# Kernel tuning notes

Hardware: AMD Instinct MI355X
Metric: run time of the kernel (lower is better)

Reference implementation:

```python
import jax, jax.numpy as jnp
import numpy as np

S, N, V, E, H, L = 40, 256, 32000, 1024, 1024, 2


def _gru_step(x, h, wih, whh, bih, bhh):
    # PyTorch GRU cell, gate order [r, z, n]
    gi = x @ wih.T + bih          # (N, 3H)
    gh = h @ whh.T + bhh          # (N, 3H)
    ir, iz, inn = jnp.split(gi, 3, axis=-1)
    hr, hz, hn = jnp.split(gh, 3, axis=-1)
    r = jax.nn.sigmoid(ir + hr)
    z = jax.nn.sigmoid(iz + hz)
    n = jnp.tanh(inn + r * hn)
    return (1.0 - z) * n + z * h


def setup_inputs() -> dict:
    key = jax.random.key(0)
    ks = jax.random.split(key, 16)
    nrm = lambda k, shp: (jax.random.normal(k, shp, jnp.float32) * 0.05)
    return {
        "tokens": jax.random.randint(ks[0], (S, N), 0, V),
        "hidden": jnp.zeros((L, N, H), jnp.float32),
        "emb": nrm(ks[1], (V, E)),
        "enc_wih": nrm(ks[2], (L, 3 * H, E)),
        "enc_whh": nrm(ks[3], (L, 3 * H, H)),
        "enc_bih": nrm(ks[4], (L, 3 * H)),
        "enc_bhh": nrm(ks[5], (L, 3 * H)),
        "dec_wih": nrm(ks[6], (L, 3 * H, H)),
        "dec_whh": nrm(ks[7], (L, 3 * H, H)),
        "dec_bih": nrm(ks[8], (L, 3 * H)),
        "dec_bhh": nrm(ks[9], (L, 3 * H)),
        "attn_w": nrm(ks[10], (S, E + L * H)),
        "attn_b": nrm(ks[11], (S,)),
        "comb_w": nrm(ks[12], (H, 2 * H)),
        "comb_b": nrm(ks[13], (H,)),
    }


def reference(tokens, hidden, emb, enc_wih, enc_whh, enc_bih, enc_bhh,
              dec_wih, dec_whh, dec_bih, dec_bhh,
              attn_w, attn_b, comb_w, comb_b):
    x = emb[tokens]                      # (S, N, E) embedded input

    # ---- encoder: 2-layer GRU over the full sequence ----
    seq = x
    h_finals = []
    for l in range(L):
        wih, whh, bih, bhh = enc_wih[l], enc_whh[l], enc_bih[l], enc_bhh[l]
        def step(h, xt, wih=wih, whh=whh, bih=bih, bhh=bhh):
            h2 = _gru_step(xt, h, wih, whh, bih, bhh)
            return h2, h2
        hT, seq = jax.lax.scan(step, hidden[l], seq)
        h_finals.append(hT)
    h_n = jnp.stack(h_finals)            # (L, N, H)
    enc_out = jnp.swapaxes(seq, 0, 1)    # (N, S, H)

    # ---- attention decoder: scan over timesteps, carry decoder hidden ----
    def dec_step(h, emb_t):
        # h: (L, N, H), emb_t: (N, E)
        h_flat = jnp.swapaxes(h, 0, 1).reshape(N, L * H)
        logits = jnp.concatenate([emb_t, h_flat], axis=-1) @ attn_w.T + attn_b
        aw = jax.nn.softmax(logits, axis=-1)                   # (N, S)
        applied = jnp.einsum('ns,nsh->nh', aw, enc_out)        # (N, H)
        xcur = jax.nn.relu(
            jnp.concatenate([emb_t, applied], axis=-1) @ comb_w.T + comb_b)
        hs = []
        for l in range(L):
            hl = _gru_step(xcur, h[l], dec_wih[l], dec_whh[l],
                           dec_bih[l], dec_bhh[l])
            hs.append(hl)
            xcur = hl
        return jnp.stack(hs), xcur

    hT, outs = jax.lax.scan(dec_step, h_n, x)   # outs: (S, N, H)
    return outs, hT
```

## Files before the change

kernel.cpp:

```cpp
#include <hip/hip_runtime.h>
#include <hip/hip_bf16.h>

#define S_LEN 40
#define NB    256
#define EDIM  1024
#define HDIM  1024
#define NBLK  256
#define NTHR  768

typedef _Float16 f16;
typedef __attribute__((ext_vector_type(8))) _Float16 f16x8;
typedef __attribute__((ext_vector_type(4))) _Float16 f16x4;
typedef __attribute__((ext_vector_type(4))) float f32x4;

__device__ __forceinline__ float sigm(float x) {
    x = fminf(fmaxf(x, -30.f), 30.f);
    return 1.f / (1.f + __expf(-x));
}
__device__ __forceinline__ float tanh_fast(float x) {
    x = fminf(fmaxf(x, -15.f), 15.f);
    float e = __expf(2.f * x);
    return (e - 1.f) / (e + 1.f);
}

__device__ __forceinline__ void sysld_issue_b128(f16x8& v, const void* p) {
    asm volatile("global_load_dwordx4 %0, %1, off sc0 sc1" : "=v"(v) : "v"(p));
}
__device__ __forceinline__ void sysld_issue_f32(float& v, const void* p) {
    asm volatile("global_load_dword %0, %1, off sc0 sc1" : "=v"(v) : "v"(p));
}
__device__ __forceinline__ void sysld_issue_f32x4(f32x4& v, const void* p) {
    asm volatile("global_load_dwordx4 %0, %1, off sc0 sc1" : "=v"(v) : "v"(p));
}
__device__ __forceinline__ void sys_wait() {
    asm volatile("s_waitcnt vmcnt(0)" ::: "memory");
    __builtin_amdgcn_sched_barrier(0);
}
__device__ __forceinline__ void sysst_f32(float* p, float v) {
    asm volatile("global_store_dword %0, %1, off sc0 sc1" :: "v"(p), "v"(v) : "memory");
}
__device__ __forceinline__ void sysst_f32x4(float* p, f32x4 v) {
    asm volatile("global_store_dwordx4 %0, %1, off sc0 sc1" :: "v"(p), "v"(v) : "memory");
}
__device__ __forceinline__ void sysst_f16(f16* p, f16 v) {
    union { f16 f; unsigned short s; } u; u.f = v;
    unsigned int b = u.s;
    asm volatile("global_store_short %0, %1, off sc0 sc1" :: "v"(p), "v"(b) : "memory");
}

__device__ __forceinline__ void gbar(unsigned* cnt, unsigned* gen) {
    asm volatile("s_waitcnt vmcnt(0)" ::: "memory");
    __syncthreads();
    if (threadIdx.x == 0) {
        unsigned g = __hip_atomic_load(gen, __ATOMIC_RELAXED, __HIP_MEMORY_SCOPE_AGENT);
        unsigned a = __hip_atomic_fetch_add(cnt, 1u, __ATOMIC_RELEASE, __HIP_MEMORY_SCOPE_AGENT);
        if (a == NBLK - 1) {
            __hip_atomic_store(cnt, 0u, __ATOMIC_RELAXED, __HIP_MEMORY_SCOPE_AGENT);
            __hip_atomic_fetch_add(gen, 1u, __ATOMIC_RELEASE, __HIP_MEMORY_SCOPE_AGENT);
        } else {
            while (__hip_atomic_load(gen, __ATOMIC_RELAXED, __HIP_MEMORY_SCOPE_AGENT) == g)
                __builtin_amdgcn_s_sleep(2);
        }
    }
    __syncthreads();
}

__global__ void k_init_sync(unsigned* s) { s[0] = 0; s[1] = 0; }

__device__ __forceinline__ void probe_mn(int lane, int* mrow, int* ncol) {
    f16x8 pa, pb;
#pragma unroll
    for (int e = 0; e < 8; e++) {
        pa[e] = (f16)(float)(lane & 15);
        pb[e] = (f16)0.03125f;
    }
    f32x4 pacc = {0, 0, 0, 0};
    pacc = __builtin_amdgcn_mfma_f32_16x16x32_f16(pa, pb, pacc, 0, 0, 0);
#pragma unroll
    for (int r = 0; r < 4; r++) {
        int m = (int)(pacc[r] + 0.5f);
        int cg = ((lane >> 4) << 2) + r;
        mrow[r] = m;
        ncol[r] = (m == cg) ? (lane & 15) : cg;
    }
}

__global__ __launch_bounds__(256) void k_cvt4(const float* __restrict__ src,
                                              f16* __restrict__ dst, int n4) {
    int i = blockIdx.x * 256 + threadIdx.x;
    if (i < n4) {
        f32x4 v = ((const f32x4*)src)[i];
        f16x4 o = {(f16)v.x, (f16)v.y, (f16)v.z, (f16)v.w};
        ((f16x4*)dst)[i] = o;
    }
}
__global__ __launch_bounds__(256) void k_copyf4(const float* __restrict__ src,
                                                float* __restrict__ dst, int n4) {
    int i = blockIdx.x * 256 + threadIdx.x;
    if (i < n4) ((f32x4*)dst)[i] = ((const f32x4*)src)[i];
}
__global__ __launch_bounds__(256) void k_embed_cvt(const int* __restrict__ tok,
                                                   const float* __restrict__ emb,
                                                   f16* __restrict__ xe) {
    int b = blockIdx.x;
    int t = threadIdx.x;
    int token = tok[b];
    f32x4 v = ((const f32x4*)(emb + (size_t)token * EDIM))[t];
    f16x4 o = {(f16)v.x, (f16)v.y, (f16)v.z, (f16)v.w};
    ((f16x4*)(xe + (size_t)b * EDIM))[t] = o;
}

__device__ void gru_phase(
    char* lds, int bid, int tid, const int* mr, const int* nc,
    const f16* __restrict__ xsrc, bool xsys,
    const f16* __restrict__ hsrc, const float* __restrict__ hfsrc,
    const f16* __restrict__ wih, const f16* __restrict__ whh,
    const float* __restrict__ bih, const float* __restrict__ bhh,
    f16* ho16, float* hof, f16* o216, float* o2f) {
    const int cb = (bid & 31) * 32;
    const int rb = (bid >> 5) * 32;

    {
        constexpr int TOT = 8192;
        constexpr int IT = (TOT + NTHR - 1) / NTHR;
        f16x8 val[IT];
#pragma unroll
        for (int i = 0; i < IT; i++) {
            int c = tid + i * NTHR;
            if (c < TOT) {
                int isH = c >> 12;
                int cl = c & 4095;
                int row = cl >> 7, cc = cl & 127;
                const f16* src = (isH ? hsrc : xsrc) +
                                 (size_t)(rb + row) * 1024 + cc * 8;
                if (isH || xsys) sysld_issue_b128(val[i], src);
                else             val[i] = *(const f16x8*)src;
            }
        }
        sys_wait();
#pragma unroll
        for (int i = 0; i < IT; i++) {
            int c = tid + i * NTHR;
            if (c < TOT) {
                int isH = c >> 12;
                int cl = c & 4095;
                int row = cl >> 7, cc = cl & 127;
                *(f16x8*)(lds + isH * 65536 + row * 2048 +
                          ((cc ^ (row & 7)) << 4)) = val[i];
            }
        }
    }
    __syncthreads();

    const int w = tid >> 6, lane = tid & 63;
    const int pair = w >> 1, kh = w & 1;
    const int gate = (pair >= 3) ? pair - 3 : pair;
    const int r0 = lane & 15, kk0 = (lane >> 4) * 8;
    const f16* B = ((pair < 3) ? wih : whh) + ((size_t)gate * HDIM + cb) * 1024;
    const f16* B0 = B + (size_t)r0 * 1024 + kk0 + kh * 512;
    const f16* B1 = B + (size_t)(r0 + 16) * 1024 + kk0 + kh * 512;
    const int abase = (pair < 3) ? 0 : 65536;
    const int swz = r0 & 7;
    const char* a0p = lds + abase + r0 * 2048;
    const char* a1p = lds + abase + (r0 + 16) * 2048;

    f32x4 acc00 = {0,0,0,0}, acc01 = {0,0,0,0}, acc10 = {0,0,0,0}, acc11 = {0,0,0,0};
#pragma unroll 4
    for (int k = 0; k < 512; k += 32) {
        int g = (kh * 512 + kk0 + k) >> 3;
        int off = (g ^ swz) << 4;
        f16x8 a0 = *(const f16x8*)(a0p + off);
        f16x8 a1 = *(const f16x8*)(a1p + off);
        f16x8 b0 = *(const f16x8*)(B0 + k);
        f16x8 b1 = *(const f16x8*)(B1 + k);
        acc00 = __builtin_amdgcn_mfma_f32_16x16x32_f16(a0, b0, acc00, 0, 0, 0);
        acc01 = __builtin_amdgcn_mfma_f32_16x16x32_f16(a0, b1, acc01, 0, 0, 0);
        acc10 = __builtin_amdgcn_mfma_f32_16x16x32_f16(a1, b0, acc10, 0, 0, 0);
        acc11 = __builtin_amdgcn_mfma_f32_16x16x32_f16(a1, b1, acc11, 0, 0, 0);
    }
    __syncthreads();

    float* red = (float*)lds;
    float* rw = red + w * 1024;
#pragma unroll
    for (int r = 0; r < 4; r++) {
        rw[mr[r] * 32 + nc[r]]             = acc00[r];
        rw[mr[r] * 32 + nc[r] + 16]        = acc01[r];
        rw[(mr[r] + 16) * 32 + nc[r]]      = acc10[r];
        rw[(mr[r] + 16) * 32 + nc[r] + 16] = acc11[r];
    }
    __syncthreads();

    {
        float hp[2];
#pragma unroll
        for (int it = 0; it < 2; it++) {
            int i = tid + it * NTHR;
            if (i < 1024) {
                int rr = i >> 5, ccn = i & 31;
                sysld_issue_f32(hp[it], hfsrc + (size_t)(rb + rr) * HDIM + cb + ccn);
            }
        }
        sys_wait();
#pragma unroll
        for (int it = 0; it < 2; it++) {
            int i = tid + it * NTHR;
            if (i < 1024) {
                int rr = i >> 5, ccn = i & 31;
                int col = cb + ccn;
                int row = rb + rr;
                float gir = red[i]         + red[1024 + i];
                float giz = red[2048 + i]  + red[3072 + i];
                float gin = red[4096 + i]  + red[5120 + i];
                float ghr = red[6144 + i]  + red[7168 + i];
                float ghz = red[8192 + i]  + red[9216 + i];
                float ghn = red[10240 + i] + red[11264 + i];
                float r = sigm(gir + bih[col] + ghr + bhh[col]);
                float z = sigm(giz + bih[HDIM + col] + ghz + bhh[HDIM + col]);
                float n = tanh_fast(gin + bih[2 * HDIM + col] +
                                    r * (ghn + bhh[2 * HDIM + col]));
                float hn2 = (1.f - z) * n + z * hp[it];
                size_t idx = (size_t)row * HDIM + col;
                sysst_f16(ho16 + idx, (f16)hn2);
                sysst_f32(hof + idx, hn2);
                if (o216) sysst_f16(o216 + idx, (f16)hn2);
                if (o2f)  sysst_f32(o2f + idx, hn2);
            }
        }
    }
}

__device__ void attn_phase(
    char* lds, int bid, int tid,
    const f16* __restrict__ xe_t, const f16* __restrict__ h0,
    const f16* __restrict__ h1,
    const f16* __restrict__ attn_w, const float* __restrict__ attn_b,
    const f16* __restrict__ enc16, f16* __restrict__ appl) {
    float* logit = (float*)(lds + 131072);
    float* awls  = logit + 64;
    const int n = bid;
    const int w = tid >> 6, lane = tid & 63;

    {
        constexpr int TOT = 5504;
        constexpr int IT = (TOT + NTHR - 1) / NTHR;
        f16x8 val[IT];
#pragma unroll
        for (int i = 0; i < IT; i++) {
            int c = tid + i * NTHR;
            if (c < TOT) {
                if (c < 5120) {
                    int s = c >> 7, cc = c & 127;
                    val[i] = *(const f16x8*)(enc16 + ((size_t)s * NB + n) * 1024 + cc * 8);
                } else {
                    int r = c - 5120;
                    if (r < 128) {
                        val[i] = *(const f16x8*)(xe_t + (size_t)n * 1024 + r * 8);
                    } else if (r < 256) {
                        sysld_issue_b128(val[i], h0 + (size_t)n * 1024 + (r - 128) * 8);
                    } else {
                        sysld_issue_b128(val[i], h1 + (size_t)n * 1024 + (r - 256) * 8);
                    }
                }
            }
        }
        sys_wait();
#pragma unroll
        for (int i = 0; i < IT; i++) {
            int c = tid + i * NTHR;
            if (c < TOT) {
                if (c < 5120) *(f16x8*)(lds + c * 16) = val[i];
                else          *(f16x8*)(lds + 81920 + (c - 5120) * 16) = val[i];
            }
        }
    }
    __syncthreads();

    if (w < 10) {
#pragma unroll
        for (int si = 0; si < 4; si++) {
            int s = w * 4 + si;
            const f16* wrow = attn_w + (size_t)s * 3072;
            float acc = 0.f;
#pragma unroll
            for (int jj = 0; jj < 6; jj++) {
                int j = lane + jj * 64;
                f16x8 a = *(const f16x8*)(lds + 81920 + j * 16);
                f16x8 b = *(const f16x8*)(wrow + j * 8);
#pragma unroll
                for (int e = 0; e < 8; e++)
                    acc = fmaf((float)a[e], (float)b[e], acc);
            }
            for (int o = 32; o; o >>= 1) acc += __shfl_down(acc, o);
            if (lane == 0) logit[s] = acc + attn_b[s];
        }
    }
    __syncthreads();

    if (w == 0) {
        float v = (lane < S_LEN) ? logit[lane] : -1e30f;
        float m = v;
        for (int o = 32; o; o >>= 1) m = fmaxf(m, __shfl_xor(m, o));
        float e = (lane < S_LEN) ? __expf(v - m) : 0.f;
        float sum = e;
        for (int o = 32; o; o >>= 1) sum += __shfl_xor(sum, o);
        if (lane < S_LEN) awls[lane] = e / sum;
    }
    __syncthreads();

    for (int col = tid; col < 1024; col += NTHR) {
        float acc = 0.f;
#pragma unroll
        for (int s = 0; s < S_LEN; s++)
            acc = fmaf(awls[s], (float)*(const f16*)(lds + s * 2048 + col * 2), acc);
        sysst_f16(appl + (size_t)n * 1024 + col, (f16)acc);
    }
}

__device__ void comb_phase(
    char* lds, int bid, int tid, const int* mr, const int* nc,
    const f16* __restrict__ xe_t, const f16* __restrict__ appl,
    const f16* __restrict__ Bw, const float* __restrict__ bias,
    f16* __restrict__ Cout) {
    const int cb = (bid & 31) * 32;
    const int rb = (bid >> 5) * 32;

    {
        constexpr int TOT = 8192;
        constexpr int IT = (TOT + NTHR - 1) / NTHR;
        f16x8 val[IT];
#pragma unroll
        for (int i = 0; i < IT; i++) {
            int c = tid + i * NTHR;
            if (c < TOT) {
                int row = c >> 8, cc = c & 255;
                if (cc < 128)
                    val[i] = *(const f16x8*)(xe_t + (size_t)(rb + row) * 1024 + cc * 8);
                else
                    sysld_issue_b128(val[i], appl + (size_t)(rb + row) * 1024 + (cc - 128) * 8);
            }
        }
        sys_wait();
#pragma unroll
        for (int i = 0; i < IT; i++) {
            int c = tid + i * NTHR;
            if (c < TOT) {
                int row = c >> 8, cc = c & 255;
                *(f16x8*)(lds + row * 4096 + ((cc ^ (row & 7)) << 4)) = val[i];
            }
        }
    }
    __syncthreads();

    const int w = tid >> 6, lane = tid & 63;
    const int r0 = lane & 15, kk0 = (lane >> 4) * 8;
    const int c0 = (w * 64) / 12, c1 = ((w + 1) * 64) / 12;
    const f16* B0 = Bw + (size_t)(cb + r0) * 2048 + kk0;
    const f16* B1 = Bw + (size_t)(cb + r0 + 16) * 2048 + kk0;
    const int swz = r0 & 7;
    const char* a0p = lds + r0 * 4096;
    const char* a1p = lds + (r0 + 16) * 4096;

    f32x4 acc00 = {0,0,0,0}, acc01 = {0,0,0,0}, acc10 = {0,0,0,0}, acc11 = {0,0,0,0};
    for (int c = c0; c < c1; c++) {
        int g = (c * 32 + kk0) >> 3;
        int off = (g ^ swz) << 4;
        f16x8 a0 = *(const f16x8*)(a0p + off);
        f16x8 a1 = *(const f16x8*)(a1p + off);
        f16x8 b0 = *(const f16x8*)(B0 + c * 32);
        f16x8 b1 = *(const f16x8*)(B1 + c * 32);
        acc00 = __builtin_amdgcn_mfma_f32_16x16x32_f16(a0, b0, acc00, 0, 0, 0);
        acc01 = __builtin_amdgcn_mfma_f32_16x16x32_f16(a0, b1, acc01, 0, 0, 0);
        acc10 = __builtin_amdgcn_mfma_f32_16x16x32_f16(a1, b0, acc10, 0, 0, 0);
        acc11 = __builtin_amdgcn_mfma_f32_16x16x32_f16(a1, b1, acc11, 0, 0, 0);
    }
    __syncthreads();

    float* red = (float*)lds;
    float* rw = red + w * 1024;
#pragma unroll
    for (int r = 0; r < 4; r++) {
        rw[mr[r] * 32 + nc[r]]             = acc00[r];
        rw[mr[r] * 32 + nc[r] + 16]        = acc01[r];
        rw[(mr[r] + 16) * 32 + nc[r]]      = acc10[r];
        rw[(mr[r] + 16) * 32 + nc[r] + 16] = acc11[r];
    }
    __syncthreads();

#pragma unroll
    for (int it = 0; it < 2; it++) {
        int i = tid + it * NTHR;
        if (i < 1024) {
            float s = 0.f;
#pragma unroll
            for (int p = 0; p < 12; p++) s += red[p * 1024 + i];
            int rr = i >> 5, ccn = i & 31;
            s += bias[cb + ccn];
            s = fmaxf(s, 0.f);
            sysst_f16(Cout + (size_t)(rb + rr) * 1024 + cb + ccn, (f16)s);
        }
    }
}

__global__ __launch_bounds__(NTHR, 3) void k_mega(
    const f16* __restrict__ xe,
    f16* h16, float* hf,
    const f16* __restrict__ w_eih, const f16* __restrict__ w_ehh,
    const float* __restrict__ enc_bih, const float* __restrict__ enc_bhh,
    const f16* __restrict__ w_dih, const f16* __restrict__ w_dhh,
    const float* __restrict__ dec_bih, const float* __restrict__ dec_bhh,
    const f16* __restrict__ w_attn, const float* __restrict__ attn_b,
    const f16* __restrict__ w_comb, const float* __restrict__ comb_b,
    f16* enc16, f16* appl, f16* xcur,
    float* out, unsigned* sync) {
    __shared__ char smem[131584];
    char* lds = smem;
    const int bid = blockIdx.x;
    const int tid = threadIdx.x;
    const int lane = tid & 63;
    const size_t NH = (size_t)NB * HDIM;

    int mr[4], nc[4];
    probe_mn(lane, mr, nc);

    unsigned* cnt = sync;
    unsigned* gen = sync + 1;

    f16* h0b[2] = { h16, h16 + 2 * NH };
    f16* h1b[2] = { h16 + NH, h16 + 3 * NH };
    float* h0f[2] = { hf, hf + 2 * NH };
    float* h1f[2] = { hf + NH, hf + 3 * NH };

    for (int t = 0; t < S_LEN; t++) {
        int p = t & 1;
        gru_phase(lds, bid, tid, mr, nc,
                  xe + (size_t)t * NB * EDIM, false,
                  h0b[p], h0f[p],
                  w_eih, w_ehh, enc_bih, enc_bhh,
                  h0b[p ^ 1], h0f[p ^ 1], (f16*)nullptr, (float*)nullptr);
        gbar(cnt, gen);
        gru_phase(lds, bid, tid, mr, nc,
                  h0b[p ^ 1], true,
                  h1b[p], h1f[p],
                  w_eih + (size_t)3 * HDIM * EDIM, w_ehh + (size_t)3 * HDIM * HDIM,
                  enc_bih + 3 * HDIM, enc_bhh + 3 * HDIM,
                  h1b[p ^ 1], h1f[p ^ 1], enc16 + (size_t)t * NH, (float*)nullptr);
        gbar(cnt, gen);
    }

    for (int t = 0; t < S_LEN; t++) {
        int p = t & 1;
        attn_phase(lds, bid, tid,
                   xe + (size_t)t * NB * EDIM, h0b[p], h1b[p],
                   w_attn, attn_b, enc16, appl);
        gbar(cnt, gen);
        comb_phase(lds, bid, tid, mr, nc,
                   xe + (size_t)t * NB * EDIM, appl, w_comb, comb_b, xcur);
        gbar(cnt, gen);
        gru_phase(lds, bid, tid, mr, nc,
                  xcur, true,
                  h0b[p], h0f[p],
                  w_dih, w_dhh, dec_bih, dec_bhh,
                  h0b[p ^ 1], h0f[p ^ 1], (f16*)nullptr, (float*)nullptr);
        gbar(cnt, gen);
        gru_phase(lds, bid, tid, mr, nc,
                  h0b[p ^ 1], true,
                  h1b[p], h1f[p],
                  w_dih + (size_t)3 * HDIM * HDIM, w_dhh + (size_t)3 * HDIM * HDIM,
                  dec_bih + 3 * HDIM, dec_bhh + 3 * HDIM,
                  h1b[p ^ 1], h1f[p ^ 1], (f16*)nullptr, out + (size_t)t * NH);
        gbar(cnt, gen);
    }

    if (tid < 512) {
        size_t idx = (size_t)bid * 512 + tid;
        f32x4 v;
        sysld_issue_f32x4(v, hf + idx * 4);
        sys_wait();
        sysst_f32x4(out + (size_t)S_LEN * NH + idx * 4, v);
    }
}

extern "C" void kernel_launch(void* const* d_in, const int* in_sizes, int n_in,
                              void* d_out, int out_size, void* d_ws, size_t ws_size,
                              hipStream_t stream) {
    const int*   tokens   = (const int*)d_in[0];
    const float* hidden   = (const float*)d_in[1];
    const float* emb      = (const float*)d_in[2];
    const float* enc_wih  = (const float*)d_in[3];
    const float* enc_whh  = (const float*)d_in[4];
    const float* enc_bih  = (const float*)d_in[5];
    const float* enc_bhh  = (const float*)d_in[6];
    const float* dec_wih  = (const float*)d_in[7];
    const float* dec_whh  = (const float*)d_in[8];
    const float* dec_bih  = (const float*)d_in[9];
    const float* dec_bhh  = (const float*)d_in[10];
    const float* attn_w   = (const float*)d_in[11];
    const float* attn_b   = (const float*)d_in[12];
    const float* comb_w   = (const float*)d_in[13];
    const float* comb_b   = (const float*)d_in[14];
    float* out = (float*)d_out;

    const size_t NH = (size_t)NB * HDIM;
    const size_t WSZ = (size_t)2 * 3 * HDIM * EDIM;

    float* hf = (float*)d_ws;
    f16* wp = (f16*)(hf + 4 * NH);
    f16 *w_eih = wp;  wp += WSZ;
    f16 *w_ehh = wp;  wp += WSZ;
    f16 *w_dih = wp;  wp += WSZ;
    f16 *w_dhh = wp;  wp += WSZ;
    f16 *w_comb = wp; wp += (size_t)HDIM * 2048;
    f16 *w_attn = wp; wp += (size_t)S_LEN * 3072;
    f16 *xe = wp;     wp += (size_t)S_LEN * NB * EDIM;
    f16 *enc16 = wp;  wp += (size_t)S_LEN * NH;
    f16 *h16 = wp;    wp += 4 * NH;
    f16 *appl = wp;   wp += NH;
    f16 *xcur = wp;   wp += NH;
    unsigned* syncp = (unsigned*)((((uintptr_t)wp) + 255) & ~(uintptr_t)255);

    k_init_sync<<<1, 1, 0, stream>>>(syncp);

    k_cvt4<<<(int)(WSZ / 4 / 256), 256, 0, stream>>>(enc_wih, w_eih, (int)(WSZ / 4));
    k_cvt4<<<(int)(WSZ / 4 / 256), 256, 0, stream>>>(enc_whh, w_ehh, (int)(WSZ / 4));
    k_cvt4<<<(int)(WSZ / 4 / 256), 256, 0, stream>>>(dec_wih, w_dih, (int)(WSZ / 4));
    k_cvt4<<<(int)(WSZ / 4 / 256), 256, 0, stream>>>(dec_whh, w_dhh, (int)(WSZ / 4));
    k_cvt4<<<(int)(HDIM * 2048 / 4 / 256), 256, 0, stream>>>(comb_w, w_comb,
                                                             HDIM * 2048 / 4);
    k_cvt4<<<(S_LEN * 3072 / 4 + 255) / 256, 256, 0, stream>>>(attn_w, w_attn,
                                                               S_LEN * 3072 / 4);
    k_embed_cvt<<<S_LEN * NB, 256, 0, stream>>>(tokens, emb, xe);
    k_cvt4<<<(int)(2 * NH / 4 / 256), 256, 0, stream>>>(hidden, h16, (int)(2 * NH / 4));
    k_copyf4<<<(int)(2 * NH / 4 / 256), 256, 0, stream>>>(hidden, hf, (int)(2 * NH / 4));

    k_mega<<<NBLK, NTHR, 0, stream>>>(
        xe, h16, hf,
        w_eih, w_ehh, enc_bih, enc_bhh,
        w_dih, w_dhh, dec_bih, dec_bhh,
        w_attn, attn_b, w_comb, comb_b,
        enc16, appl, xcur, out, syncp);
}
```

Baseline: 6.495 ms.

## Use hierarchical per-XCD grid barrier and nontemporal system-scope loads/stores

The flat global barrier, where all 256 blocks hit one counter, becomes a two-level barrier. Blocks first arrive on a counter for their own XCD, read from the hardware register, and then one representative per XCD arrives on a global counter. Per-XCD block counts are found at startup with an extra bootstrap barrier. All system-scope loads and stores gain the nt hint, and the encoder-output reads in attention now use sc0 sc1 loads, so data written by other XCDs is seen coherently. The aim is less atomic contention per barrier, at the cost of a second atomic hop and more complex startup logic.

```diff
diff --git a/kernel.cpp b/kernel.cpp
--- a/kernel.cpp
+++ b/kernel.cpp
@@ -24,31 +24,31 @@
 }
 
 __device__ __forceinline__ void sysld_issue_b128(f16x8& v, const void* p) {
-    asm volatile("global_load_dwordx4 %0, %1, off sc0 sc1" : "=v"(v) : "v"(p));
+    asm volatile("global_load_dwordx4 %0, %1, off sc0 sc1 nt" : "=v"(v) : "v"(p));
 }
 __device__ __forceinline__ void sysld_issue_f32(float& v, const void* p) {
-    asm volatile("global_load_dword %0, %1, off sc0 sc1" : "=v"(v) : "v"(p));
+    asm volatile("global_load_dword %0, %1, off sc0 sc1 nt" : "=v"(v) : "v"(p));
 }
 __device__ __forceinline__ void sysld_issue_f32x4(f32x4& v, const void* p) {
-    asm volatile("global_load_dwordx4 %0, %1, off sc0 sc1" : "=v"(v) : "v"(p));
+    asm volatile("global_load_dwordx4 %0, %1, off sc0 sc1 nt" : "=v"(v) : "v"(p));
 }
 __device__ __forceinline__ void sys_wait() {
     asm volatile("s_waitcnt vmcnt(0)" ::: "memory");
     __builtin_amdgcn_sched_barrier(0);
 }
 __device__ __forceinline__ void sysst_f32(float* p, float v) {
-    asm volatile("global_store_dword %0, %1, off sc0 sc1" :: "v"(p), "v"(v) : "memory");
+    asm volatile("global_store_dword %0, %1, off sc0 sc1 nt" :: "v"(p), "v"(v) : "memory");
 }
 __device__ __forceinline__ void sysst_f32x4(float* p, f32x4 v) {
-    asm volatile("global_store_dwordx4 %0, %1, off sc0 sc1" :: "v"(p), "v"(v) : "memory");
+    asm volatile("global_store_dwordx4 %0, %1, off sc0 sc1 nt" :: "v"(p), "v"(v) : "memory");
 }
 __device__ __forceinline__ void sysst_f16(f16* p, f16 v) {
     union { f16 f; unsigned short s; } u; u.f = v;
     unsigned int b = u.s;
-    asm volatile("global_store_short %0, %1, off sc0 sc1" :: "v"(p), "v"(b) : "memory");
-}
-
-__device__ __forceinline__ void gbar(unsigned* cnt, unsigned* gen) {
+    asm volatile("global_store_short %0, %1, off sc0 sc1 nt" :: "v"(p), "v"(b) : "memory");
+}
+
+__device__ __forceinline__ void gbar1(unsigned* cnt, unsigned* gen) {
     asm volatile("s_waitcnt vmcnt(0)" ::: "memory");
     __syncthreads();
     if (threadIdx.x == 0) {
@@ -65,7 +65,37 @@
     __syncthreads();
 }
 
-__global__ void k_init_sync(unsigned* s) { s[0] = 0; s[1] = 0; }
+__device__ __forceinline__ void g2bar(unsigned* sync, unsigned xcd,
+                                      unsigned M, unsigned NX) {
+    asm volatile("s_waitcnt vmcnt(0)" ::: "memory");
+    __syncthreads();
+    if (threadIdx.x == 0) {
+        unsigned* ggen = sync;
+        unsigned* gcnt = sync + 1;
+        unsigned* xa = sync + 16 + xcd * 16;
+        unsigned g = __hip_atomic_load(ggen, __ATOMIC_RELAXED, __HIP_MEMORY_SCOPE_AGENT);
+        unsigned a = __hip_atomic_fetch_add(xa, 1u, __ATOMIC_RELEASE, __HIP_MEMORY_SCOPE_AGENT);
+        if (a == M - 1) {
+            __hip_atomic_store(xa, 0u, __ATOMIC_RELAXED, __HIP_MEMORY_SCOPE_AGENT);
+            unsigned b = __hip_atomic_fetch_add(gcnt, 1u, __ATOMIC_RELEASE, __HIP_MEMORY_SCOPE_AGENT);
+            if (b == NX - 1) {
+                __hip_atomic_store(gcnt, 0u, __ATOMIC_RELAXED, __HIP_MEMORY_SCOPE_AGENT);
+                __hip_atomic_fetch_add(ggen, 1u, __ATOMIC_RELEASE, __HIP_MEMORY_SCOPE_AGENT);
+            } else {
+                while (__hip_atomic_load(ggen, __ATOMIC_RELAXED, __HIP_MEMORY_SCOPE_AGENT) == g)
+                    __builtin_amdgcn_s_sleep(4);
+            }
+        } else {
+            while (__hip_atomic_load(ggen, __ATOMIC_RELAXED, __HIP_MEMORY_SCOPE_AGENT) == g)
+                __builtin_amdgcn_s_sleep(4);
+        }
+    }
+    __syncthreads();
+}
+
+__global__ void k_init_sync(unsigned* s) {
+    for (int k = threadIdx.x; k < 1024; k += 256) s[k] = 0;
+}
 
 __device__ __forceinline__ void probe_mn(int lane, int* mrow, int* ncol) {
     f16x8 pa, pb;
@@ -251,7 +281,7 @@
             if (c < TOT) {
                 if (c < 5120) {
                     int s = c >> 7, cc = c & 127;
-                    val[i] = *(const f16x8*)(enc16 + ((size_t)s * NB + n) * 1024 + cc * 8);
+                    sysld_issue_b128(val[i], enc16 + ((size_t)s * NB + n) * 1024 + cc * 8);
                 } else {
                     int r = c - 5120;
                     if (r < 128) {
@@ -414,6 +444,7 @@
     f16* enc16, f16* appl, f16* xcur,
     float* out, unsigned* sync) {
     __shared__ char smem[131584];
+    __shared__ unsigned s_meta[4];
     char* lds = smem;
     const int bid = blockIdx.x;
     const int tid = threadIdx.x;
@@ -423,8 +454,27 @@
     int mr[4], nc[4];
     probe_mn(lane, mr, nc);
 
-    unsigned* cnt = sync;
-    unsigned* gen = sync + 1;
+    if (tid == 0) {
+        unsigned x;
+        asm volatile("s_getreg_b32 %0, hwreg(20, 0, 32)" : "=s"(x));
+        x &= 7;
+        unsigned r = __hip_atomic_fetch_add(sync + 256 + x, 1u,
+                                            __ATOMIC_RELAXED, __HIP_MEMORY_SCOPE_AGENT);
+        s_meta[0] = x; s_meta[1] = r;
+    }
+    __syncthreads();
+    gbar1(sync + 512, sync + 513);
+    if (tid == 0) {
+        unsigned M = __hip_atomic_load(sync + 256 + s_meta[0],
+                                       __ATOMIC_RELAXED, __HIP_MEMORY_SCOPE_AGENT);
+        unsigned nx = 0;
+        for (int i = 0; i < 8; i++)
+            nx += (__hip_atomic_load(sync + 256 + i, __ATOMIC_RELAXED,
+                                     __HIP_MEMORY_SCOPE_AGENT) > 0) ? 1u : 0u;
+        s_meta[2] = M; s_meta[3] = nx;
+    }
+    __syncthreads();
+    const unsigned xcd = s_meta[0], M = s_meta[2], NX = s_meta[3];
 
     f16* h0b[2] = { h16, h16 + 2 * NH };
     f16* h1b[2] = { h16 + NH, h16 + 3 * NH };
@@ -438,14 +488,14 @@
                   h0b[p], h0f[p],
                   w_eih, w_ehh, enc_bih, enc_bhh,
                   h0b[p ^ 1], h0f[p ^ 1], (f16*)nullptr, (float*)nullptr);
-        gbar(cnt, gen);
+        g2bar(sync, xcd, M, NX);
         gru_phase(lds, bid, tid, mr, nc,
                   h0b[p ^ 1], true,
                   h1b[p], h1f[p],
                   w_eih + (size_t)3 * HDIM * EDIM, w_ehh + (size_t)3 * HDIM * HDIM,
                   enc_bih + 3 * HDIM, enc_bhh + 3 * HDIM,
                   h1b[p ^ 1], h1f[p ^ 1], enc16 + (size_t)t * NH, (float*)nullptr);
-        gbar(cnt, gen);
+        g2bar(sync, xcd, M, NX);
     }
 
     for (int t = 0; t < S_LEN; t++) {
@@ -453,23 +503,23 @@
         attn_phase(lds, bid, tid,
                    xe + (size_t)t * NB * EDIM, h0b[p], h1b[p],
                    w_attn, attn_b, enc16, appl);
-        gbar(cnt, gen);
+        g2bar(sync, xcd, M, NX);
         comb_phase(lds, bid, tid, mr, nc,
                    xe + (size_t)t * NB * EDIM, appl, w_comb, comb_b, xcur);
-        gbar(cnt, gen);
+        g2bar(sync, xcd, M, NX);
         gru_phase(lds, bid, tid, mr, nc,
                   xcur, true,
                   h0b[p], h0f[p],
                   w_dih, w_dhh, dec_bih, dec_bhh,
                   h0b[p ^ 1], h0f[p ^ 1], (f16*)nullptr, (float*)nullptr);
-        gbar(cnt, gen);
+        g2bar(sync, xcd, M, NX);
         gru_phase(lds, bid, tid, mr, nc,
                   h0b[p ^ 1], true,
                   h1b[p], h1f[p],
                   w_dih + (size_t)3 * HDIM * HDIM, w_dhh + (size_t)3 * HDIM * HDIM,
                   dec_bih + 3 * HDIM, dec_bhh + 3 * HDIM,
                   h1b[p ^ 1], h1f[p ^ 1], (f16*)nullptr, out + (size_t)t * NH);
-        gbar(cnt, gen);
+        g2bar(sync, xcd, M, NX);
     }
 
     if (tid < 512) {
@@ -519,7 +569,7 @@
     f16 *xcur = wp;   wp += NH;
     unsigned* syncp = (unsigned*)((((uintptr_t)wp) + 255) & ~(uintptr_t)255);
 
-    k_init_sync<<<1, 1, 0, stream>>>(syncp);
+    k_init_sync<<<1, 256, 0, stream>>>(syncp);
 
     k_cvt4<<<(int)(WSZ / 4 / 256), 256, 0, stream>>>(enc_wih, w_eih, (int)(WSZ / 4));
     k_cvt4<<<(int)(WSZ / 4 / 256), 256, 0, stream>>>(enc_whh, w_ehh, (int)(WSZ / 4));
```

Result: slower. 6.680 ms (+2.9%).
